# Kernel optimization log

Hardware: AMD Instinct MI355X
Metric: run time of the kernel (lower is better)

Reference implementation:

```python
import jax, jax.numpy as jnp
import numpy as np

NUM_HEADS = 8


def setup_inputs() -> dict:
    key = jax.random.key(0)
    ks = jax.random.split(key, 9)
    B, S, E = 16, 2048, 768
    s = 0.02
    return {
        "features": jax.random.normal(ks[0], (B, S, E), jnp.float32),
        "in_proj_w": jax.random.normal(ks[1], (3 * E, E), jnp.float32) * s,
        "in_proj_b": jnp.zeros((3 * E,), jnp.float32),
        "out_proj_w": jax.random.normal(ks[2], (E, E), jnp.float32) * s,
        "out_proj_b": jnp.zeros((E,), jnp.float32),
        "w1": jax.random.normal(ks[3], (384, E), jnp.float32) * s,
        "b1": jnp.zeros((384,), jnp.float32),
        "w2": jax.random.normal(ks[4], (1, 384), jnp.float32) * s,
        "b2": jnp.zeros((1,), jnp.float32),
    }


def reference(features, in_proj_w, in_proj_b, out_proj_w, out_proj_b, w1, b1, w2, b2):
    # torch nn.MultiheadAttention default batch_first=False: dim 0 is the
    # attended sequence axis (length B here), dim 1 is the MHA batch (S).
    B, S, E = features.shape
    H = NUM_HEADS
    Dh = E // H
    qkv = features @ in_proj_w.T + in_proj_b          # (B, S, 3E)
    q, k, v = jnp.split(qkv, 3, axis=-1)
    q = q.reshape(B, S, H, Dh)
    k = k.reshape(B, S, H, Dh)
    v = v.reshape(B, S, H, Dh)
    scale = 1.0 / jnp.sqrt(jnp.asarray(Dh, features.dtype))
    # attention over axis-0 positions (l, m in 0..B-1), per (s, h)
    scores = jnp.einsum('lshd,mshd->shlm', q * scale, k)
    attn = jax.nn.softmax(scores, axis=-1)
    ctx = jnp.einsum('shlm,mshd->lshd', attn, v).reshape(B, S, E)
    attn_out = ctx @ out_proj_w.T + out_proj_b        # (B, S, E)
    # batched 2-layer MLP (replaces the Python per-row loop)
    h = jax.nn.relu(attn_out @ w1.T + b1)             # (B, S, 384)
    prob = h @ w2.T + b2                              # (B, S, 1)
    contacts = jnp.broadcast_to(prob, (B, S, S))      # contacts[:, i, :] = prob[:, i]
    return contacts
```

## Files before the change

kernel.cpp:

```cpp
#include <hip/hip_runtime.h>

typedef unsigned short u16;
typedef __attribute__((ext_vector_type(8))) __bf16 bf16x8;
typedef __attribute__((ext_vector_type(4))) float floatx4;

#define B_DIM  16
#define S_DIM  2048
#define E_DIM  768
#define HEADS  8
#define DHEAD  96
#define MROWS  32768
#define QKV_LD 2304
#define ATT_ST 392

__device__ __forceinline__ u16 f2b(float f) {
    unsigned u = __float_as_uint(f);
    u += 0x7fffu + ((u >> 16) & 1u);
    return (u16)(u >> 16);
}
__device__ __forceinline__ float blo(unsigned u) { return __uint_as_float(u << 16); }
__device__ __forceinline__ float bhi(unsigned u) { return __uint_as_float(u & 0xffff0000u); }

__device__ __forceinline__ void axpy8(float* acc, float p, uint4 v) {
    acc[0] += p * blo(v.x); acc[1] += p * bhi(v.x);
    acc[2] += p * blo(v.y); acc[3] += p * bhi(v.y);
    acc[4] += p * blo(v.z); acc[5] += p * bhi(v.z);
    acc[6] += p * blo(v.w); acc[7] += p * bhi(v.w);
}

__global__ __launch_bounds__(256) void cvt_bf16(const float* __restrict__ in,
                                                u16* __restrict__ out, int n4) {
    int i = blockIdx.x * 256 + threadIdx.x;
    if (i < n4) {
        float4 f = ((const float4*)in)[i];
        ushort4 r;
        r.x = f2b(f.x); r.y = f2b(f.y); r.z = f2b(f.z); r.w = f2b(f.w);
        ((ushort4*)out)[i] = r;
    }
}

__global__ __launch_bounds__(256) void transpose_cvt(const float* __restrict__ in,
                                                     u16* __restrict__ out) {
    __shared__ float t[32][33];
    const int tx = threadIdx.x & 31, ty = threadIdx.x >> 5;
    int x = blockIdx.x * 32 + tx;
    int y = blockIdx.y * 32 + ty;
#pragma unroll
    for (int j = 0; j < 4; j++) t[ty + j * 8][tx] = in[(long)(y + j * 8) * 768 + x];
    __syncthreads();
    x = blockIdx.y * 32 + tx;
    y = blockIdx.x * 32 + ty;
#pragma unroll
    for (int j = 0; j < 4; j++) out[(long)(y + j * 8) * 768 + x] = f2b(t[tx][ty + j * 8]);
}

__global__ __launch_bounds__(64) void cbias_kernel(const float* __restrict__ w1,
                                                   const float* __restrict__ bo,
                                                   const float* __restrict__ b1,
                                                   float* __restrict__ c) {
    const int n = blockIdx.x * 64 + threadIdx.x;
    if (n < 384) {
        float s = b1[n];
        const float* row = w1 + (long)n * 768;
        for (int e = 0; e < 768; e++) s += row[e] * bo[e];
        c[n] = s;
    }
}

template<bool OUTF32, bool PERM, bool SWIZ>
__global__ __launch_bounds__(256) void gemm_bt(const u16* __restrict__ A, int lda,
                                               const u16* __restrict__ W,
                                               const float* __restrict__ bias,
                                               void* __restrict__ Cout, int ldc,
                                               int N, int K) {
    __shared__ __align__(16) u16 sA[128 * 32];
    __shared__ __align__(16) u16 sB[128 * 32];
    const int tid  = threadIdx.x;
    int bn, bm;
    if (SWIZ) {
        const int bx = blockIdx.x;
        bn = bx >> 8;
        bm = ((bx & 7) << 5) | ((bx >> 3) & 31);
    } else {
        bn = blockIdx.x;
        bm = blockIdx.y;
    }
    const int lane = tid & 63;
    const int wid  = tid >> 6;
    const int wm   = (wid >> 1) * 64;
    const int wn   = (wid & 1) * 64;
    const int ar = tid >> 2;
    const int ac = (tid & 3) * 8;
    const u16* Ap = A + (long)(bm * 128 + ar) * lda + ac;
    const u16* Wp = W + (long)(bn * 128 + ar) * K + ac;
    const long a2 = (long)64 * lda;
    const long w2 = (long)64 * K;

    floatx4 acc[4][4] = {};
    const int fr = lane & 15;
    const int fq = (lane >> 4) * 8;

    for (int k0 = 0; k0 < K; k0 += 32) {
        __builtin_amdgcn_global_load_lds((const __attribute__((address_space(1))) void*)(Ap + k0),
                                         (__attribute__((address_space(3))) void*)(sA + tid * 8), 16, 0, 0);
        __builtin_amdgcn_global_load_lds((const __attribute__((address_space(1))) void*)(Ap + a2 + k0),
                                         (__attribute__((address_space(3))) void*)(sA + 2048 + tid * 8), 16, 0, 0);
        __builtin_amdgcn_global_load_lds((const __attribute__((address_space(1))) void*)(Wp + k0),
                                         (__attribute__((address_space(3))) void*)(sB + tid * 8), 16, 0, 0);
        __builtin_amdgcn_global_load_lds((const __attribute__((address_space(1))) void*)(Wp + w2 + k0),
                                         (__attribute__((address_space(3))) void*)(sB + 2048 + tid * 8), 16, 0, 0);
        __syncthreads();

        bf16x8 aF[4], bF[4];
#pragma unroll
        for (int i = 0; i < 4; i++) {
            aF[i] = *(const bf16x8*)(sA + (wm + i * 16 + fr) * 32 + fq);
            bF[i] = *(const bf16x8*)(sB + (wn + i * 16 + fr) * 32 + fq);
        }
#pragma unroll
        for (int i = 0; i < 4; i++)
#pragma unroll
            for (int j = 0; j < 4; j++)
                acc[i][j] = __builtin_amdgcn_mfma_f32_16x16x32_bf16(aF[i], bF[j], acc[i][j], 0, 0, 0);
        __syncthreads();
    }

    const int rq = (lane >> 4) * 4;
#pragma unroll
    for (int i = 0; i < 4; i++) {
#pragma unroll
        for (int j = 0; j < 4; j++) {
            const int row0 = bm * 128 + wm + i * 16 + rq;
            const int col  = bn * 128 + wn + j * 16 + fr;
            const float bv = bias[col];
#pragma unroll
            for (int r = 0; r < 4; r++) {
                float v = acc[i][j][r] + bv;
                const int rl = row0 + r;
                const long grow = PERM ? (long)(((rl & 2047) << 4) | (rl >> 11)) : (long)rl;
                if (OUTF32) ((float*)Cout)[grow * ldc + col] = v;
                else        ((u16*)Cout)[grow * ldc + col]   = f2b(v);
            }
        }
    }
}

__global__ __launch_bounds__(256) void attn_kernel(u16* __restrict__ qkv) {
    __shared__ __align__(16) u16 sQ[16 * ATT_ST], sK[16 * ATT_ST], sV[16 * ATT_ST];
    __shared__ float sS[4][16][16];
    const int tid = threadIdx.x;
    const int s  = blockIdx.x >> 1;
    const int hh = blockIdx.x & 1;
    const u16* base = qkv + (long)s * 16 * QKV_LD + hh * 384;

#pragma unroll
    for (int it = 0; it < 9; it++) {
        const int i = it * 256 + tid;
        const int t = i / 768, rem = i % 768, l = rem / 48, c = rem % 48;
        const u16* src = base + (long)l * QKV_LD + t * E_DIM + c * 8;
        u16* dst = (t == 0 ? sQ : t == 1 ? sK : sV) + l * ATT_ST + c * 8;
        *(uint4*)dst = *(const uint4*)src;
    }
    __syncthreads();

    const int lane = tid & 63;
    const int w    = tid >> 6;
    const int fr   = lane & 15;
    const int fq   = (lane >> 4) * 8;
    floatx4 acc = {};
    const u16* qrow = sQ + fr * ATT_ST + w * DHEAD + fq;
    const u16* krow = sK + fr * ATT_ST + w * DHEAD + fq;
#pragma unroll
    for (int st = 0; st < 3; st++) {
        bf16x8 qa = *(const bf16x8*)(qrow + st * 32);
        bf16x8 kb = *(const bf16x8*)(krow + st * 32);
        acc = __builtin_amdgcn_mfma_f32_16x16x32_bf16(qa, kb, acc, 0, 0, 0);
    }
    const int rq = (lane >> 4) * 4;
#pragma unroll
    for (int r = 0; r < 4; r++) {
        float sc = acc[r] * 0.10206207261596577f;
        float mx = sc;
#pragma unroll
        for (int off = 8; off > 0; off >>= 1) mx = fmaxf(mx, __shfl_xor(mx, off));
        float e = __expf(sc - mx);
        float sum = e;
#pragma unroll
        for (int off = 8; off > 0; off >>= 1) sum += __shfl_xor(sum, off);
        sS[w][rq + r][fr] = e / sum;
    }
    __syncthreads();

#pragma unroll
    for (int j = 0; j < 3; j++) {
        const int task = j * 256 + tid;
        const int h = task / 192, rem = task % 192, ll = rem / 12, c = rem % 12;
        float a[8] = {};
#pragma unroll
        for (int mm = 0; mm < 16; mm++) {
            const float p = sS[h][ll][mm];
            uint4 vw = *(const uint4*)(sV + mm * ATT_ST + h * DHEAD + c * 8);
            axpy8(a, p, vw);
        }
        ushort4 o0, o1;
        o0.x = f2b(a[0]); o0.y = f2b(a[1]); o0.z = f2b(a[2]); o0.w = f2b(a[3]);
        o1.x = f2b(a[4]); o1.y = f2b(a[5]); o1.z = f2b(a[6]); o1.w = f2b(a[7]);
        u16* dst = qkv + ((long)s * 16 + ll) * QKV_LD + (hh * 4 + h) * DHEAD + c * 8;
        *(ushort4*)dst = o0;
        *(ushort4*)(dst + 4) = o1;
    }
}

__global__ __launch_bounds__(256) void mlp_fused(const u16* __restrict__ A, int lda,
                                                 const u16* __restrict__ G,
                                                 const float* __restrict__ cbias,
                                                 const float* __restrict__ w2,
                                                 const float* __restrict__ b2,
                                                 float* __restrict__ out) {
    __shared__ __align__(16) u16 sA[128 * 32];
    __shared__ __align__(16) u16 sB[128 * 32];
    __shared__ float rowsum[128];
    const int tid = threadIdx.x;
    const int bm  = blockIdx.x;
    if (tid < 128) rowsum[tid] = 0.f;
    const int lane = tid & 63;
    const int wid  = tid >> 6;
    const int wm   = (wid >> 1) * 64;
    const int wn   = (wid & 1) * 64;
    const int ar = tid >> 2;
    const int ac = (tid & 3) * 8;
    const u16* Ap = A + (long)(bm * 128 + ar) * lda + ac;
    const long a2 = (long)64 * lda;
    const int fr = lane & 15;
    const int fq = (lane >> 4) * 8;
    const int rq = (lane >> 4) * 4;

    for (int bn = 0; bn < 3; bn++) {
        const u16* Wp = G + (long)(bn * 128 + ar) * 768 + ac;
        floatx4 acc[4][4] = {};
        for (int k0 = 0; k0 < 768; k0 += 32) {
            __builtin_amdgcn_global_load_lds((const __attribute__((address_space(1))) void*)(Ap + k0),
                                             (__attribute__((address_space(3))) void*)(sA + tid * 8), 16, 0, 0);
            __builtin_amdgcn_global_load_lds((const __attribute__((address_space(1))) void*)(Ap + a2 + k0),
                                             (__attribute__((address_space(3))) void*)(sA + 2048 + tid * 8), 16, 0, 0);
            __builtin_amdgcn_global_load_lds((const __attribute__((address_space(1))) void*)(Wp + k0),
                                             (__attribute__((address_space(3))) void*)(sB + tid * 8), 16, 0, 0);
            __builtin_amdgcn_global_load_lds((const __attribute__((address_space(1))) void*)(Wp + (long)64 * 768 + k0),
                                             (__attribute__((address_space(3))) void*)(sB + 2048 + tid * 8), 16, 0, 0);
            __syncthreads();
            bf16x8 aF[4], bF[4];
#pragma unroll
            for (int i = 0; i < 4; i++) {
                aF[i] = *(const bf16x8*)(sA + (wm + i * 16 + fr) * 32 + fq);
                bF[i] = *(const bf16x8*)(sB + (wn + i * 16 + fr) * 32 + fq);
            }
#pragma unroll
            for (int i = 0; i < 4; i++)
#pragma unroll
                for (int j = 0; j < 4; j++)
                    acc[i][j] = __builtin_amdgcn_mfma_f32_16x16x32_bf16(aF[i], bF[j], acc[i][j], 0, 0, 0);
            __syncthreads();
        }
        float part[4][4] = {};
#pragma unroll
        for (int j = 0; j < 4; j++) {
            const int col = bn * 128 + wn + j * 16 + fr;
            const float cv = cbias[col];
            const float wv = w2[col];
#pragma unroll
            for (int i = 0; i < 4; i++)
#pragma unroll
                for (int r = 0; r < 4; r++)
                    part[i][r] += fmaxf(acc[i][j][r] + cv, 0.f) * wv;
        }
#pragma unroll
        for (int i = 0; i < 4; i++)
#pragma unroll
            for (int r = 0; r < 4; r++) {
                float v = part[i][r];
#pragma unroll
                for (int off = 8; off > 0; off >>= 1) v += __shfl_xor(v, off);
                if (fr == 0) atomicAdd(&rowsum[wm + i * 16 + rq + r], v);
            }
    }
    __syncthreads();
    const float b2v = b2[0];
    for (int rr = 0; rr < 128; rr++) {
        const float pv = rowsum[rr] + b2v;
        const int p_ = bm * 128 + rr;
        float4* dst = (float4*)(out + ((long)(p_ & 15) * S_DIM + (p_ >> 4)) * S_DIM);
        float4 v4 = make_float4(pv, pv, pv, pv);
        dst[tid] = v4;
        dst[tid + 256] = v4;
    }
}

extern "C" void kernel_launch(void* const* d_in, const int* in_sizes, int n_in,
                              void* d_out, int out_size, void* d_ws, size_t ws_size,
                              hipStream_t stream) {
    const float* features   = (const float*)d_in[0];
    const float* in_proj_b  = (const float*)d_in[2];
    const float* out_proj_b = (const float*)d_in[4];
    const float* b1 = (const float*)d_in[6];
    const float* w2 = (const float*)d_in[7];
    const float* b2 = (const float*)d_in[8];
    float* out = (float*)d_out;

    char* p = (char*)d_ws;
    u16* fbf = (u16*)p; p += (size_t)MROWS * E_DIM * 2;
    u16* wib = (u16*)p; p += (size_t)QKV_LD * E_DIM * 2;
    u16* w1b = (u16*)p; p += (size_t)384 * E_DIM * 2;
    u16* WoT = (u16*)p; p += (size_t)E_DIM * E_DIM * 2;
    u16* Gbf = (u16*)p; p += (size_t)384 * E_DIM * 2;
    float* cbuf  = (float*)p; p += 384 * 4;
    float* zeros = (float*)p; p += 768 * 4;
    p = (char*)(((size_t)p + 255) & ~(size_t)255);
    u16* qkv = (u16*)p; p += (size_t)MROWS * QKV_LD * 2;
    u16* ctx = qkv;

    hipMemsetAsync(zeros, 0, 768 * 4, stream);

    cvt_bf16<<<(MROWS * E_DIM / 4 + 255) / 256, 256, 0, stream>>>(features, fbf, MROWS * E_DIM / 4);
    cvt_bf16<<<(QKV_LD * E_DIM / 4 + 255) / 256, 256, 0, stream>>>((const float*)d_in[1], wib, QKV_LD * E_DIM / 4);
    cvt_bf16<<<(384 * E_DIM / 4 + 255) / 256, 256, 0, stream>>>((const float*)d_in[5], w1b, 384 * E_DIM / 4);
    transpose_cvt<<<dim3(24, 24), 256, 0, stream>>>((const float*)d_in[3], WoT);
    cbias_kernel<<<6, 64, 0, stream>>>((const float*)d_in[5], out_proj_b, b1, cbuf);

    gemm_bt<false, false, false><<<dim3(6, 3), 256, 0, stream>>>(
        w1b, E_DIM, WoT, zeros, Gbf, E_DIM, E_DIM, E_DIM);
    gemm_bt<false, true, true><<<dim3(4608), 256, 0, stream>>>(
        fbf, E_DIM, wib, in_proj_b, qkv, QKV_LD, QKV_LD, E_DIM);
    attn_kernel<<<S_DIM * 2, 256, 0, stream>>>(qkv);
    mlp_fused<<<256, 256, 0, stream>>>(ctx, QKV_LD, Gbf, cbuf, w2, b2, out);
}
```

Baseline: 663.8 us.

## Split fused MLP into column-parallel GEMM plus separate broadcast kernel

```diff
diff --git a/kernel.cpp b/kernel.cpp
--- a/kernel.cpp
+++ b/kernel.cpp
@@ -54,17 +54,19 @@
     for (int j = 0; j < 4; j++) out[(long)(y + j * 8) * 768 + x] = f2b(t[tx][ty + j * 8]);
 }
 
-__global__ __launch_bounds__(64) void cbias_kernel(const float* __restrict__ w1,
-                                                   const float* __restrict__ bo,
-                                                   const float* __restrict__ b1,
-                                                   float* __restrict__ c) {
-    const int n = blockIdx.x * 64 + threadIdx.x;
-    if (n < 384) {
-        float s = b1[n];
-        const float* row = w1 + (long)n * 768;
-        for (int e = 0; e < 768; e++) s += row[e] * bo[e];
-        c[n] = s;
-    }
+__global__ __launch_bounds__(256) void cbias_kernel(const float* __restrict__ w1,
+                                                    const float* __restrict__ bo,
+                                                    const float* __restrict__ b1,
+                                                    float* __restrict__ c) {
+    __shared__ float red[4];
+    const int n = blockIdx.x, tid = threadIdx.x;
+    const float* row = w1 + (long)n * 768;
+    float s = row[tid] * bo[tid] + row[tid + 256] * bo[tid + 256] + row[tid + 512] * bo[tid + 512];
+#pragma unroll
+    for (int off = 32; off > 0; off >>= 1) s += __shfl_xor(s, off);
+    if ((tid & 63) == 0) red[tid >> 6] = s;
+    __syncthreads();
+    if (tid == 0) c[n] = red[0] + red[1] + red[2] + red[3] + b1[n];
 }
 
 template<bool OUTF32, bool PERM, bool SWIZ>
@@ -211,17 +213,17 @@
     }
 }
 
-__global__ __launch_bounds__(256) void mlp_fused(const u16* __restrict__ A, int lda,
-                                                 const u16* __restrict__ G,
-                                                 const float* __restrict__ cbias,
-                                                 const float* __restrict__ w2,
-                                                 const float* __restrict__ b2,
-                                                 float* __restrict__ out) {
+__global__ __launch_bounds__(256) void mlp_gemm(const u16* __restrict__ A, int lda,
+                                                const u16* __restrict__ G,
+                                                const float* __restrict__ cbias,
+                                                const float* __restrict__ w2,
+                                                float* __restrict__ part) {
     __shared__ __align__(16) u16 sA[128 * 32];
     __shared__ __align__(16) u16 sB[128 * 32];
     __shared__ float rowsum[128];
     const int tid = threadIdx.x;
-    const int bm  = blockIdx.x;
+    const int bm  = blockIdx.x / 3;
+    const int bn  = blockIdx.x % 3;
     if (tid < 128) rowsum[tid] = 0.f;
     const int lane = tid & 63;
     const int wid  = tid >> 6;
@@ -230,65 +232,72 @@
     const int ar = tid >> 2;
     const int ac = (tid & 3) * 8;
     const u16* Ap = A + (long)(bm * 128 + ar) * lda + ac;
+    const u16* Wp = G + (long)(bn * 128 + ar) * 768 + ac;
     const long a2 = (long)64 * lda;
     const int fr = lane & 15;
     const int fq = (lane >> 4) * 8;
     const int rq = (lane >> 4) * 4;
 
-    for (int bn = 0; bn < 3; bn++) {
-        const u16* Wp = G + (long)(bn * 128 + ar) * 768 + ac;
-        floatx4 acc[4][4] = {};
-        for (int k0 = 0; k0 < 768; k0 += 32) {
-            __builtin_amdgcn_global_load_lds((const __attribute__((address_space(1))) void*)(Ap + k0),
-                                             (__attribute__((address_space(3))) void*)(sA + tid * 8), 16, 0, 0);
-            __builtin_amdgcn_global_load_lds((const __attribute__((address_space(1))) void*)(Ap + a2 + k0),
-                                             (__attribute__((address_space(3))) void*)(sA + 2048 + tid * 8), 16, 0, 0);
-            __builtin_amdgcn_global_load_lds((const __attribute__((address_space(1))) void*)(Wp + k0),
-                                             (__attribute__((address_space(3))) void*)(sB + tid * 8), 16, 0, 0);
-            __builtin_amdgcn_global_load_lds((const __attribute__((address_space(1))) void*)(Wp + (long)64 * 768 + k0),
-                                             (__attribute__((address_space(3))) void*)(sB + 2048 + tid * 8), 16, 0, 0);
-            __syncthreads();
-            bf16x8 aF[4], bF[4];
-#pragma unroll
-            for (int i = 0; i < 4; i++) {
-                aF[i] = *(const bf16x8*)(sA + (wm + i * 16 + fr) * 32 + fq);
-                bF[i] = *(const bf16x8*)(sB + (wn + i * 16 + fr) * 32 + fq);
-            }
-#pragma unroll
-            for (int i = 0; i < 4; i++)
-#pragma unroll
-                for (int j = 0; j < 4; j++)
-                    acc[i][j] = __builtin_amdgcn_mfma_f32_16x16x32_bf16(aF[i], bF[j], acc[i][j], 0, 0, 0);
-            __syncthreads();
-        }
-        float part[4][4] = {};
-#pragma unroll
-        for (int j = 0; j < 4; j++) {
-            const int col = bn * 128 + wn + j * 16 + fr;
-            const float cv = cbias[col];
-            const float wv = w2[col];
-#pragma unroll
-            for (int i = 0; i < 4; i++)
-#pragma unroll
-                for (int r = 0; r < 4; r++)
-                    part[i][r] += fmaxf(acc[i][j][r] + cv, 0.f) * wv;
+    floatx4 acc[4][4] = {};
+    for (int k0 = 0; k0 < 768; k0 += 32) {
+        __builtin_amdgcn_global_load_lds((const __attribute__((address_space(1))) void*)(Ap + k0),
+                                         (__attribute__((address_space(3))) void*)(sA + tid * 8), 16, 0, 0);
+        __builtin_amdgcn_global_load_lds((const __attribute__((address_space(1))) void*)(Ap + a2 + k0),
+                                         (__attribute__((address_space(3))) void*)(sA + 2048 + tid * 8), 16, 0, 0);
+        __builtin_amdgcn_global_load_lds((const __attribute__((address_space(1))) void*)(Wp + k0),
+                                         (__attribute__((address_space(3))) void*)(sB + tid * 8), 16, 0, 0);
+        __builtin_amdgcn_global_load_lds((const __attribute__((address_space(1))) void*)(Wp + (long)64 * 768 + k0),
+                                         (__attribute__((address_space(3))) void*)(sB + 2048 + tid * 8), 16, 0, 0);
+        __syncthreads();
+        bf16x8 aF[4], bF[4];
+#pragma unroll
+        for (int i = 0; i < 4; i++) {
+            aF[i] = *(const bf16x8*)(sA + (wm + i * 16 + fr) * 32 + fq);
+            bF[i] = *(const bf16x8*)(sB + (wn + i * 16 + fr) * 32 + fq);
         }
 #pragma unroll
         for (int i = 0; i < 4; i++)
 #pragma unroll
-            for (int r = 0; r < 4; r++) {
-                float v = part[i][r];
-#pragma unroll
-                for (int off = 8; off > 0; off >>= 1) v += __shfl_xor(v, off);
-                if (fr == 0) atomicAdd(&rowsum[wm + i * 16 + rq + r], v);
-            }
-    }
-    __syncthreads();
+            for (int j = 0; j < 4; j++)
+                acc[i][j] = __builtin_amdgcn_mfma_f32_16x16x32_bf16(aF[i], bF[j], acc[i][j], 0, 0, 0);
+        __syncthreads();
+    }
+    float partl[4][4] = {};
+#pragma unroll
+    for (int j = 0; j < 4; j++) {
+        const int col = bn * 128 + wn + j * 16 + fr;
+        const float cv = cbias[col];
+        const float wv = w2[col];
+#pragma unroll
+        for (int i = 0; i < 4; i++)
+#pragma unroll
+            for (int r = 0; r < 4; r++)
+                partl[i][r] += fmaxf(acc[i][j][r] + cv, 0.f) * wv;
+    }
+#pragma unroll
+    for (int i = 0; i < 4; i++)
+#pragma unroll
+        for (int r = 0; r < 4; r++) {
+            float v = partl[i][r];
+#pragma unroll
+            for (int off = 8; off > 0; off >>= 1) v += __shfl_xor(v, off);
+            if (fr == 0) atomicAdd(&rowsum[wm + i * 16 + rq + r], v);
+        }
+    __syncthreads();
+    if (tid < 128) part[(long)bn * MROWS + bm * 128 + tid] = rowsum[tid];
+}
+
+__global__ __launch_bounds__(256) void bcast_kernel(const float* __restrict__ part,
+                                                    const float* __restrict__ b2,
+                                                    float* __restrict__ out) {
+    const int tid = threadIdx.x;
+    const long p0 = (long)blockIdx.x * 4;
     const float b2v = b2[0];
-    for (int rr = 0; rr < 128; rr++) {
-        const float pv = rowsum[rr] + b2v;
-        const int p_ = bm * 128 + rr;
-        float4* dst = (float4*)(out + ((long)(p_ & 15) * S_DIM + (p_ >> 4)) * S_DIM);
+#pragma unroll
+    for (int r = 0; r < 4; r++) {
+        const long p = p0 + r;
+        const float pv = part[p] + part[MROWS + p] + part[2 * MROWS + p] + b2v;
+        float4* dst = (float4*)(out + ((p & 15) * S_DIM + (p >> 4)) * S_DIM);
         float4 v4 = make_float4(pv, pv, pv, pv);
         dst[tid] = v4;
         dst[tid + 256] = v4;
@@ -313,6 +322,7 @@
     u16* WoT = (u16*)p; p += (size_t)E_DIM * E_DIM * 2;
     u16* Gbf = (u16*)p; p += (size_t)384 * E_DIM * 2;
     float* cbuf  = (float*)p; p += 384 * 4;
+    float* partb = (float*)p; p += (size_t)3 * MROWS * 4;
     float* zeros = (float*)p; p += 768 * 4;
     p = (char*)(((size_t)p + 255) & ~(size_t)255);
     u16* qkv = (u16*)p; p += (size_t)MROWS * QKV_LD * 2;
@@ -324,12 +334,13 @@
     cvt_bf16<<<(QKV_LD * E_DIM / 4 + 255) / 256, 256, 0, stream>>>((const float*)d_in[1], wib, QKV_LD * E_DIM / 4);
     cvt_bf16<<<(384 * E_DIM / 4 + 255) / 256, 256, 0, stream>>>((const float*)d_in[5], w1b, 384 * E_DIM / 4);
     transpose_cvt<<<dim3(24, 24), 256, 0, stream>>>((const float*)d_in[3], WoT);
-    cbias_kernel<<<6, 64, 0, stream>>>((const float*)d_in[5], out_proj_b, b1, cbuf);
+    cbias_kernel<<<384, 256, 0, stream>>>((const float*)d_in[5], out_proj_b, b1, cbuf);
 
     gemm_bt<false, false, false><<<dim3(6, 3), 256, 0, stream>>>(
         w1b, E_DIM, WoT, zeros, Gbf, E_DIM, E_DIM, E_DIM);
     gemm_bt<false, true, true><<<dim3(4608), 256, 0, stream>>>(
         fbf, E_DIM, wib, in_proj_b, qkv, QKV_LD, QKV_LD, E_DIM);
     attn_kernel<<<S_DIM * 2, 256, 0, stream>>>(qkv);
-    mlp_fused<<<256, 256, 0, stream>>>(ctx, QKV_LD, Gbf, cbuf, w2, b2, out);
-}
+    mlp_gemm<<<768, 256, 0, stream>>>(ctx, QKV_LD, Gbf, cbuf, w2, partb);
+    bcast_kernel<<<MROWS / 4, 256, 0, stream>>>(partb, b2, out);
+}
```

Measured after the change: 622.1 us. 6.3% less time.
